# Kernel tuning notes

Measured on AMD Instinct MI355X. Metric: run time of the kernel, lower is better.

## Reference

```python
import jax, jax.numpy as jnp
import numpy as np
from jax import lax

EPS = 1e-8
NUM_CLASSES = 10
OUT_DIM = 16
IN_CAPS = 32 * 6 * 6  # 1152
IN_DIM = 8
NUM_ITERS = 3


def squash(x, axis=-1):
    norm = jnp.sum(x * x, axis=axis, keepdims=True)
    return norm / (norm + 1.0) * x / (jnp.sqrt(norm) + EPS)


def conv2d(x, w, b, stride):
    y = lax.conv_general_dilated(x, w, window_strides=(stride, stride), padding='VALID',
                                 dimension_numbers=('NCHW', 'OIHW', 'NCHW'))
    return y + b[None, :, None, None]


def setup_inputs() -> dict:
    key = jax.random.key(0)
    ks = jax.random.split(key, 12)
    B = 256
    inp = {}
    inp['x'] = jax.random.normal(ks[0], (B, 1, 28, 28), dtype=jnp.float32)
    inp['y'] = jax.random.randint(ks[1], (B,), 0, NUM_CLASSES)
    s = 0.05
    inp['conv1_w'] = jax.random.normal(ks[2], (256, 1, 9, 9), dtype=jnp.float32) * s
    inp['conv1_b'] = jnp.zeros((256,), dtype=jnp.float32)
    inp['prim_w'] = jax.random.normal(ks[3], (32 * 8, 256, 9, 9), dtype=jnp.float32) * s
    inp['prim_b'] = jnp.zeros((32 * 8,), dtype=jnp.float32)
    # torch init is randn; scaled down mildly for numerical sanity
    inp['route_W'] = jax.random.normal(ks[4], (NUM_CLASSES, IN_CAPS, IN_DIM, OUT_DIM), dtype=jnp.float32) * 0.1
    inp['dec_w1'] = jax.random.normal(ks[5], (NUM_CLASSES * OUT_DIM, 512), dtype=jnp.float32) * s
    inp['dec_b1'] = jnp.zeros((512,), dtype=jnp.float32)
    inp['dec_w2'] = jax.random.normal(ks[6], (512, 1024), dtype=jnp.float32) * s
    inp['dec_b2'] = jnp.zeros((1024,), dtype=jnp.float32)
    inp['dec_w3'] = jax.random.normal(ks[7], (1024, 28 * 28), dtype=jnp.float32) * s
    inp['dec_b3'] = jnp.zeros((28 * 28,), dtype=jnp.float32)
    return inp


def reference(x, y, conv1_w, conv1_b, prim_w, prim_b, route_W,
              dec_w1, dec_b1, dec_w2, dec_b2, dec_w3, dec_b3):
    B = x.shape[0]
    # conv1 + relu: [B,256,20,20]
    h = jax.nn.relu(conv2d(x, conv1_w, conv1_b, stride=1))
    # primary capsules: conv stride 2 -> [B,256,6,6] -> [B,1152,8], squash
    p = conv2d(h, prim_w, prim_b, stride=2)
    u = squash(p.reshape(B, -1, IN_DIM))  # [B,1152,8]
    # routing: u_hat [B,C,N,D]
    u_hat = jnp.einsum('bnd,cnde->bcne', u, route_W)
    b_logits = jnp.zeros_like(u_hat)
    for _ in range(NUM_ITERS - 1):
        c = jax.nn.softmax(b_logits, axis=2)
        s = jnp.sum(c * u_hat, axis=2, keepdims=True)  # [B,C,1,D]
        v = squash(s)
        b_logits = b_logits + u_hat * v
    c = jax.nn.softmax(b_logits, axis=2)
    s = jnp.sum(c * u_hat, axis=2, keepdims=True)
    v = squash(s)[:, :, 0, :]  # [B,C,D]
    logits = jax.nn.softmax(jnp.sqrt(jnp.sum(v * v, axis=-1)), axis=-1)  # [B,C]
    y_onehot = jax.nn.one_hot(y, NUM_CLASSES, dtype=v.dtype)  # [B,C]
    d = (v * y_onehot[:, :, None]).reshape(B, -1)  # [B,160]
    d = jax.nn.relu(d @ dec_w1 + dec_b1)
    d = jax.nn.relu(d @ dec_w2 + dec_b2)
    recons = d @ dec_w3 + dec_b3  # [B,784]
    return logits, recons
```

## Files before the change

### kernel.cpp

```cpp
#include <hip/hip_runtime.h>
#include <hip/hip_fp16.h>
#include <math.h>

#define EPS 1e-8f
#define AS1 __attribute__((address_space(1)))
#define AS3 __attribute__((address_space(3)))

typedef _Float16 f16x8 __attribute__((ext_vector_type(8)));
typedef float f32x4 __attribute__((ext_vector_type(4)));

__global__ __launch_bounds__(256) void transpose_k(const float* __restrict__ in,
                                                   float* __restrict__ out, int R, int C) {
    __shared__ float tile[64][65];
    int tx = threadIdx.x & 63, ty = threadIdx.x >> 6;
    int c0 = blockIdx.x * 64, r0 = blockIdx.y * 64;
#pragma unroll
    for (int i = 0; i < 16; ++i) {
        int r = r0 + ty + i * 4, c = c0 + tx;
        if (r < R && c < C) tile[ty + i * 4][tx] = in[(long)r * C + c];
    }
    __syncthreads();
#pragma unroll
    for (int i = 0; i < 16; ++i) {
        int r = c0 + ty + i * 4, c = r0 + tx;
        if (r < C && c < R) out[(long)r * R + c] = tile[tx][ty + i * 4];
    }
}

__global__ __launch_bounds__(256) void wprep_k(const float* __restrict__ prim_w,
                                               __half* __restrict__ w2) {
    __shared__ float pl[128 * 81];
    int t = threadIdx.x, co = blockIdx.x, cih = blockIdx.y;
    for (int i = t; i < 10368; i += 256) pl[i] = prim_w[co * 20736 + cih * 10368 + i];
    __syncthreads();
    for (int o = t; o < 10368; o += 256) {
        int tap = o >> 7, cil = o & 127;
        w2[(long)co * 20736 + tap * 256 + cih * 128 + cil] = __float2half(pl[cil * 81 + tap]);
    }
}

__global__ __launch_bounds__(256) void conv1_k(const float* __restrict__ x,
                                               const float* __restrict__ wt1,
                                               const float* __restrict__ bias,
                                               __half* __restrict__ hh) {
    __shared__ float img[784];
    __shared__ float wl2[81 * 128];
    int t = threadIdx.x, b = blockIdx.x;
    int chalf = blockIdx.y >> 1, ph = blockIdx.y & 1;
    for (int i = t; i < 784; i += 256) img[i] = x[b * 784 + i];
    for (int i = t; i < 81 * 128; i += 256) {
        int tap = i >> 7, j = i & 127;
        wl2[i] = wt1[tap * 256 + chalf * 128 + j];
    }
    __syncthreads();
    int lane = t & 63, grp = t >> 6;
    int col = lane * 2;
    float2 cb = *(const float2*)&bias[chalf * 128 + col];
    int ow0 = ph * 10;
    for (int oh = grp * 5; oh < grp * 5 + 5; ++oh) {
        float acc0[10], acc1[10];
#pragma unroll
        for (int p = 0; p < 10; ++p) { acc0[p] = 0.f; acc1[p] = 0.f; }
        for (int kh = 0; kh < 9; ++kh) {
            for (int kw = 0; kw < 9; ++kw) {
                float2 w2v = *(const float2*)&wl2[(kh * 9 + kw) * 128 + col];
                const float* irow = &img[(oh + kh) * 28 + ow0 + kw];
#pragma unroll
                for (int p = 0; p < 10; ++p) {
                    float iv = irow[p];
                    acc0[p] += iv * w2v.x;
                    acc1[p] += iv * w2v.y;
                }
            }
        }
#pragma unroll
        for (int p = 0; p < 10; ++p) {
            int pix = oh * 20 + ow0 + p;
            __half2 hv;
            hv.x = __float2half(fmaxf(acc0[p] + cb.x, 0.f));
            hv.y = __float2half(fmaxf(acc1[p] + cb.y, 0.f));
            *(__half2*)&hh[((long)b * 400 + pix) * 256 + chalf * 128 + col] = hv;
        }
    }
}

__global__ __launch_bounds__(256) void primgemm_k(const __half* __restrict__ hh,
                                                  const __half* __restrict__ w2,
                                                  float* __restrict__ Cpart) {
    __shared__ __align__(16) char lds[2][32768];
    const int t = threadIdx.x;
    const int lane = t & 63, w = t >> 6;
    const int l15 = lane & 15, kl = lane >> 4;
    const int sw = l15 & 7;

    const int bx = blockIdx.x;
    const int mt = bx >> 3, nb = (bx >> 2) & 1, ks = bx & 3;
    const int mr = w >> 1, nc = w & 1;

    long wsrc[4], asrc[4];
    int dstW[4];
#pragma unroll
    for (int q = 0; q < 4; ++q) {
        int row = q * 32 + w * 8 + (lane >> 3);
        int lc = (lane & 7) ^ (row & 7);
        dstW[q] = q * 4096 + w * 1024;
        wsrc[q] = (long)(nb * 128 + row) * 20736 + ks * 64 + lc * 8;
        int m = mt * 128 + row;
        int bi = m / 36, pos = m - bi * 36;
        int oy = pos / 6, ox = pos - oy * 6;
        asrc[q] = ((long)bi * 400 + oy * 40 + ox * 2) * 256 + ks * 64 + lc * 8;
    }

    f32x4 acc[4][4];
#pragma unroll
    for (int i = 0; i < 4; ++i)
#pragma unroll
        for (int j = 0; j < 4; ++j) acc[i][j] = (f32x4){0.f, 0.f, 0.f, 0.f};

    auto stage = [&](int bufi, int tap) {
        int kh = tap / 9, kw = tap - kh * 9;
        int woff = tap * 256;
        int aoff = (kh * 20 + kw) * 256;
#pragma unroll
        for (int q = 0; q < 4; ++q)
            __builtin_amdgcn_global_load_lds((const AS1 void*)(w2 + wsrc[q] + woff),
                                             (AS3 void*)(&lds[bufi][dstW[q]]), 16, 0, 0);
#pragma unroll
        for (int q = 0; q < 4; ++q)
            __builtin_amdgcn_global_load_lds((const AS1 void*)(hh + asrc[q] + aoff),
                                             (AS3 void*)(&lds[bufi][16384 + dstW[q]]), 16, 0, 0);
    };

    int wrowb[4], arowb[4], rdoff[2];
#pragma unroll
    for (int f = 0; f < 4; ++f) {
        wrowb[f] = (nc * 64 + f * 16 + l15) * 128;
        arowb[f] = 16384 + (mr * 64 + f * 16 + l15) * 128;
    }
#pragma unroll
    for (int kc = 0; kc < 2; ++kc) rdoff[kc] = ((kc * 4 + kl) ^ sw) << 4;

    stage(0, 0);
    __syncthreads();
    int buf = 0;
    for (int s = 0; s < 81; ++s) {
        if (s < 80) stage(buf ^ 1, s + 1);
        const char* B = lds[buf];
#pragma unroll
        for (int kc = 0; kc < 2; ++kc) {
            f16x8 wf[4], af[4];
#pragma unroll
            for (int nf = 0; nf < 4; ++nf) wf[nf] = *(const f16x8*)(B + wrowb[nf] + rdoff[kc]);
#pragma unroll
            for (int mf = 0; mf < 4; ++mf) af[mf] = *(const f16x8*)(B + arowb[mf] + rdoff[kc]);
#pragma unroll
            for (int mf = 0; mf < 4; ++mf)
#pragma unroll
                for (int nf = 0; nf < 4; ++nf)
                    acc[mf][nf] = __builtin_amdgcn_mfma_f32_16x16x32_f16(wf[nf], af[mf],
                                                                         acc[mf][nf], 0, 0, 0);
        }
        __syncthreads();
        buf ^= 1;
    }

    float* Cp = Cpart + (long)ks * 2359296;
#pragma unroll
    for (int mf = 0; mf < 4; ++mf)
#pragma unroll
        for (int nf = 0; nf < 4; ++nf) {
            int m = mt * 128 + mr * 64 + mf * 16 + l15;
            int co = nb * 128 + nc * 64 + nf * 16 + kl * 4;
            *(f32x4*)(Cp + (long)m * 256 + co) = acc[mf][nf];
        }
}

__global__ __launch_bounds__(256) void squashp_k(const float* __restrict__ Cpart,
                                                 const float* __restrict__ bias,
                                                 float* __restrict__ u) {
    __shared__ float sm[9216];
    __shared__ float bs[256];
    int t = threadIdx.x, b = blockIdx.x;
    bs[t] = bias[t];
    for (int i = t; i < 9216; i += 256) {
        float s = 0.f;
#pragma unroll
        for (int ks = 0; ks < 4; ++ks) s += Cpart[(long)ks * 2359296 + (long)b * 9216 + i];
        sm[i] = s;
    }
    __syncthreads();
    for (int cap = t; cap < 1152; cap += 256) {
        float xs[8], sn = 0.f;
#pragma unroll
        for (int d = 0; d < 8; ++d) {
            int f = cap * 8 + d;
            int co = f / 36, pos = f - co * 36;
            float vv = sm[pos * 256 + co] + bs[co];
            xs[d] = vv;
            sn += vv * vv;
        }
        float sc = sn / ((sn + 1.f) * (sqrtf(sn) + EPS));
#pragma unroll
        for (int d = 0; d < 8; ++d) u[(long)b * 9216 + cap * 8 + d] = xs[d] * sc;
    }
}

__global__ __launch_bounds__(256) void route_k(const float* __restrict__ u,
                                               const float* __restrict__ W,
                                               float* __restrict__ v) {
    __shared__ float red[4][18];
    int t = threadIdx.x;
    int c = blockIdx.x >> 8, b = blockIdx.x & 255;
    int lane = t & 63, w = t >> 6;
    const float* Wc = W + c * 147456;
    const float* ub = u + b * 9216;
    const float valid4 = (t < 128) ? 1.f : 0.f;

    float uh[5][16];
#pragma unroll
    for (int i = 0; i < 5; ++i) {
        int n = (i == 4) ? ((t < 128) ? 1024 + t : 0) : (t + 256 * i);
        float4 ua = *(const float4*)(ub + n * 8);
        float4 ubv = *(const float4*)(ub + n * 8 + 4);
        float ud[8] = {ua.x, ua.y, ua.z, ua.w, ubv.x, ubv.y, ubv.z, ubv.w};
#pragma unroll
        for (int e = 0; e < 16; ++e) uh[i][e] = 0.f;
#pragma unroll
        for (int d = 0; d < 8; ++d) {
            const float* wr = Wc + n * 128 + d * 16;
#pragma unroll
            for (int eq = 0; eq < 4; ++eq) {
                float4 wq = *(const float4*)(wr + eq * 4);
                uh[i][eq * 4 + 0] += ud[d] * wq.x;
                uh[i][eq * 4 + 1] += ud[d] * wq.y;
                uh[i][eq * 4 + 2] += ud[d] * wq.z;
                uh[i][eq * 4 + 3] += ud[d] * wq.w;
            }
        }
    }

    float vsum[16], sv[16];
#pragma unroll
    for (int e = 0; e < 16; ++e) vsum[e] = 0.f;

    for (int iter = 0; iter < 3; ++iter) {
        float li[5];
        float pmax = -1e30f;
#pragma unroll
        for (int i = 0; i < 5; ++i) {
            float s = 0.f;
#pragma unroll
            for (int e = 0; e < 16; ++e) s += uh[i][e] * vsum[e];
            li[i] = s;
            float sm = (i == 4 && valid4 == 0.f) ? -1e30f : s;
            pmax = fmaxf(pmax, sm);
        }
#pragma unroll
        for (int m = 1; m < 64; m <<= 1) pmax = fmaxf(pmax, __shfl_xor(pmax, m, 64));
        if (lane == 0) red[w][17] = pmax;
        __syncthreads();
        float M = fmaxf(fmaxf(red[0][17], red[1][17]), fmaxf(red[2][17], red[3][17]));

        float pe = 0.f, se[16];
#pragma unroll
        for (int e = 0; e < 16; ++e) se[e] = 0.f;
#pragma unroll
        for (int i = 0; i < 5; ++i) {
            float E = __expf(li[i] - M);
            if (i == 4) E *= valid4;
            pe += E;
#pragma unroll
            for (int e = 0; e < 16; ++e) se[e] += E * uh[i][e];
        }
#pragma unroll
        for (int m = 1; m < 64; m <<= 1) {
            pe += __shfl_xor(pe, m, 64);
#pragma unroll
            for (int e = 0; e < 16; ++e) se[e] += __shfl_xor(se[e], m, 64);
        }
        if (lane == 0) {
            red[w][16] = pe;
#pragma unroll
            for (int e = 0; e < 16; ++e) red[w][e] = se[e];
        }
        __syncthreads();
        float peT = red[0][16] + red[1][16] + red[2][16] + red[3][16];
        float rp = 1.f / peT;
        float nrm = 0.f;
#pragma unroll
        for (int e = 0; e < 16; ++e) {
            sv[e] = (red[0][e] + red[1][e] + red[2][e] + red[3][e]) * rp;
            nrm += sv[e] * sv[e];
        }
        float sc = nrm / ((nrm + 1.f) * (sqrtf(nrm) + EPS));
#pragma unroll
        for (int e = 0; e < 16; ++e) {
            sv[e] *= sc;
            vsum[e] += sv[e];
        }
    }
    if (t == 0) {
#pragma unroll
        for (int e = 0; e < 16; ++e) v[(b * 10 + c) * 16 + e] = sv[e];
    }
}

__global__ __launch_bounds__(256) void logits_k(const float* __restrict__ v,
                                                float* __restrict__ out) {
    int b = threadIdx.x;
    float nr[10];
#pragma unroll
    for (int c = 0; c < 10; ++c) {
        float s2 = 0.f;
#pragma unroll
        for (int e = 0; e < 16; ++e) {
            float xv = v[(b * 10 + c) * 16 + e];
            s2 += xv * xv;
        }
        nr[c] = sqrtf(s2);
    }
    float mx = nr[0];
#pragma unroll
    for (int c = 1; c < 10; ++c) mx = fmaxf(mx, nr[c]);
    float ex[10], sm = 0.f;
#pragma unroll
    for (int c = 0; c < 10; ++c) {
        ex[c] = __expf(nr[c] - mx);
        sm += ex[c];
    }
#pragma unroll
    for (int c = 0; c < 10; ++c) out[b * 10 + c] = ex[c] / sm;
}

__global__ __launch_bounds__(256) void fc1_k(const float* __restrict__ v,
                                             const int* __restrict__ y,
                                             const float* __restrict__ w1,
                                             const float* __restrict__ b1,
                                             float* __restrict__ h1) {
    int b = blockIdx.x, t = threadIdx.x;
    __shared__ float vs[16];
    int cls = y[b];
    if (t < 16) vs[t] = v[(b * 10 + cls) * 16 + t];
    __syncthreads();
    for (int j = t; j < 512; j += 256) {
        float a = b1[j];
#pragma unroll
        for (int d = 0; d < 16; ++d) a += vs[d] * w1[(cls * 16 + d) * 512 + j];
        h1[b * 512 + j] = fmaxf(a, 0.f);
    }
}

__global__ __launch_bounds__(256) void fc_k(const float* __restrict__ A,
                                            const float* __restrict__ Wt,
                                            const float* __restrict__ bias,
                                            float* __restrict__ C,
                                            int K, int N, int relu) {
    __shared__ float al[8 * 1024];
    int t = threadIdx.x;
    int j = blockIdx.x * 256 + t;
    int r0 = blockIdx.y * 8;
    for (int idx = t; idx < 8 * K; idx += 256) {
        int r = idx / K, kk = idx - r * K;
        al[r * K + kk] = A[(r0 + r) * K + kk];
    }
    __syncthreads();
    if (j < N) {
        float bj = bias[j];
        float acc[8];
#pragma unroll
        for (int i = 0; i < 8; ++i) acc[i] = bj;
        for (int k = 0; k < K; ++k) {
            float w = Wt[(long)k * N + j];
#pragma unroll
            for (int i = 0; i < 8; ++i) acc[i] += al[i * K + k] * w;
        }
#pragma unroll
        for (int i = 0; i < 8; ++i) {
            float o = acc[i];
            if (relu) o = fmaxf(o, 0.f);
            C[(r0 + i) * N + j] = o;
        }
    }
}

extern "C" void kernel_launch(void* const* d_in, const int* in_sizes, int n_in,
                              void* d_out, int out_size, void* d_ws, size_t ws_size,
                              hipStream_t stream) {
    (void)in_sizes; (void)n_in; (void)out_size; (void)ws_size;
    const float* x       = (const float*)d_in[0];
    const int*   y       = (const int*)d_in[1];
    const float* conv1_w = (const float*)d_in[2];
    const float* conv1_b = (const float*)d_in[3];
    const float* prim_w  = (const float*)d_in[4];
    const float* prim_b  = (const float*)d_in[5];
    const float* route_W = (const float*)d_in[6];
    const float* dec_w1  = (const float*)d_in[7];
    const float* dec_b1  = (const float*)d_in[8];
    const float* dec_w2  = (const float*)d_in[9];
    const float* dec_b2  = (const float*)d_in[10];
    const float* dec_w3  = (const float*)d_in[11];
    const float* dec_b3  = (const float*)d_in[12];
    float* out = (float*)d_out;

    float* ws  = (float*)d_ws;
    float* Cp  = ws;
    float* u   = Cp + 9437184;
    float* wt1 = u + 2359296;
    float* v   = wt1 + 20736;
    float* h1  = v + 40960;
    float* h2  = h1 + 131072;
    __half* hh = (__half*)(h2 + 262144);
    __half* w2 = hh + 26214400;

    hipLaunchKernelGGL(transpose_k, dim3(2, 4), dim3(256), 0, stream, conv1_w, wt1, 256, 81);
    hipLaunchKernelGGL(wprep_k, dim3(256, 2), dim3(256), 0, stream, prim_w, w2);
    hipLaunchKernelGGL(conv1_k, dim3(256, 4), dim3(256), 0, stream, x, wt1, conv1_b, hh);
    hipLaunchKernelGGL(primgemm_k, dim3(576), dim3(256), 0, stream, hh, w2, Cp);
    hipLaunchKernelGGL(squashp_k, dim3(256), dim3(256), 0, stream, Cp, prim_b, u);
    hipLaunchKernelGGL(route_k, dim3(2560), dim3(256), 0, stream, u, route_W, v);
    hipLaunchKernelGGL(logits_k, dim3(1), dim3(256), 0, stream, v, out);
    hipLaunchKernelGGL(fc1_k, dim3(256), dim3(256), 0, stream, v, y, dec_w1, dec_b1, h1);
    hipLaunchKernelGGL(fc_k, dim3(4, 32), dim3(256), 0, stream, h1, dec_w2, dec_b2, h2, 512, 1024, 1);
    hipLaunchKernelGGL(fc_k, dim3(4, 32), dim3(256), 0, stream, h2, dec_w3, dec_b3, out + 2560, 1024, 784, 0);
}
```

Before: 696.8 us.

## Split routing into u_hat precompute kernel with fp16 storage; register-cache conv1 rows

Routing is split in two. A new kernel computes u_hat once per (class, capsule group), keeping W in LDS and reusing it across all batch items, and writes u_hat as fp16 into the reused hh buffer. The routing kernel then just loads its fp16 u_hat slice instead of re-reading W from global memory for every batch item. Conv1 also loads each input row into 19 registers once and reuses them across kw taps instead of re-reading LDS. The costs are a 47 MB fp16 intermediate written and read through HBM, fp16 rounding of u_hat, and an extra barrier per routing iteration.

```diff
diff --git a/kernel.cpp b/kernel.cpp
--- a/kernel.cpp
+++ b/kernel.cpp
@@ -61,15 +61,19 @@
         float acc0[10], acc1[10];
 #pragma unroll
         for (int p = 0; p < 10; ++p) { acc0[p] = 0.f; acc1[p] = 0.f; }
+#pragma unroll
         for (int kh = 0; kh < 9; ++kh) {
+            float r[19];
+            const float* irow = &img[(oh + kh) * 28 + ow0];
+#pragma unroll
+            for (int q = 0; q < 19; ++q) r[q] = irow[q];
+#pragma unroll
             for (int kw = 0; kw < 9; ++kw) {
-                float2 w2v = *(const float2*)&wl2[(kh * 9 + kw) * 128 + col];
-                const float* irow = &img[(oh + kh) * 28 + ow0 + kw];
+                float2 wv = *(const float2*)&wl2[(kh * 9 + kw) * 128 + col];
 #pragma unroll
                 for (int p = 0; p < 10; ++p) {
-                    float iv = irow[p];
-                    acc0[p] += iv * w2v.x;
-                    acc1[p] += iv * w2v.y;
+                    acc0[p] += r[kw + p] * wv.x;
+                    acc1[p] += r[kw + p] * wv.y;
                 }
             }
         }
@@ -205,38 +209,69 @@
     }
 }
 
-__global__ __launch_bounds__(256) void route_k(const float* __restrict__ u,
-                                               const float* __restrict__ W,
-                                               float* __restrict__ v) {
+__global__ __launch_bounds__(256) void uhat_k(const float* __restrict__ u,
+                                              const float* __restrict__ W,
+                                              __half* __restrict__ uh) {
+    __shared__ float wl[32 * 132];
+    int t = threadIdx.x;
+    int c = blockIdx.x / 36, ng = blockIdx.x - c * 36;
+    const float* Wc = W + (long)c * 147456 + ng * 4096;
+    for (int i = t; i < 4096; i += 256) {
+        int row = i >> 7, k = i & 127;
+        wl[row * 132 + k] = Wc[i];
+    }
+    __syncthreads();
+    int nl = t >> 3, bl = t & 7;
+    int n = ng * 32 + nl;
+    const float* wr = &wl[nl * 132];
+    for (int bq = 0; bq < 32; ++bq) {
+        int b = bq * 8 + bl;
+        const float* ub = u + (long)b * 9216 + n * 8;
+        float4 ua = *(const float4*)ub, uv = *(const float4*)(ub + 4);
+        float ud[8] = {ua.x, ua.y, ua.z, ua.w, uv.x, uv.y, uv.z, uv.w};
+        float acc[16];
+#pragma unroll
+        for (int e = 0; e < 16; ++e) acc[e] = 0.f;
+#pragma unroll
+        for (int d = 0; d < 8; ++d) {
+            const float* wd = wr + d * 16;
+#pragma unroll
+            for (int eq = 0; eq < 4; ++eq) {
+                float4 wq = *(const float4*)(wd + eq * 4);
+                acc[eq * 4 + 0] += ud[d] * wq.x;
+                acc[eq * 4 + 1] += ud[d] * wq.y;
+                acc[eq * 4 + 2] += ud[d] * wq.z;
+                acc[eq * 4 + 3] += ud[d] * wq.w;
+            }
+        }
+        f16x8 o0, o1;
+#pragma unroll
+        for (int e = 0; e < 8; ++e) {
+            o0[e] = (_Float16)acc[e];
+            o1[e] = (_Float16)acc[8 + e];
+        }
+        __half* dst = uh + ((long)(c * 256 + b)) * 18432 + n * 16;
+        *(f16x8*)dst = o0;
+        *(f16x8*)(dst + 8) = o1;
+    }
+}
+
+__global__ __launch_bounds__(256) void route2_k(const __half* __restrict__ uh,
+                                                float* __restrict__ v) {
     __shared__ float red[4][18];
     int t = threadIdx.x;
     int c = blockIdx.x >> 8, b = blockIdx.x & 255;
     int lane = t & 63, w = t >> 6;
-    const float* Wc = W + c * 147456;
-    const float* ub = u + b * 9216;
     const float valid4 = (t < 128) ? 1.f : 0.f;
-
-    float uh[5][16];
+    const __half* ub = uh + ((long)(c * 256 + b)) * 18432;
+
+    f16x8 uhh[5][2];
 #pragma unroll
     for (int i = 0; i < 5; ++i) {
         int n = (i == 4) ? ((t < 128) ? 1024 + t : 0) : (t + 256 * i);
-        float4 ua = *(const float4*)(ub + n * 8);
-        float4 ubv = *(const float4*)(ub + n * 8 + 4);
-        float ud[8] = {ua.x, ua.y, ua.z, ua.w, ubv.x, ubv.y, ubv.z, ubv.w};
-#pragma unroll
-        for (int e = 0; e < 16; ++e) uh[i][e] = 0.f;
-#pragma unroll
-        for (int d = 0; d < 8; ++d) {
-            const float* wr = Wc + n * 128 + d * 16;
-#pragma unroll
-            for (int eq = 0; eq < 4; ++eq) {
-                float4 wq = *(const float4*)(wr + eq * 4);
-                uh[i][eq * 4 + 0] += ud[d] * wq.x;
-                uh[i][eq * 4 + 1] += ud[d] * wq.y;
-                uh[i][eq * 4 + 2] += ud[d] * wq.z;
-                uh[i][eq * 4 + 3] += ud[d] * wq.w;
-            }
-        }
+        const __half* p = ub + n * 16;
+        uhh[i][0] = *(const f16x8*)p;
+        uhh[i][1] = *(const f16x8*)(p + 8);
     }
 
     float vsum[16], sv[16];
@@ -250,7 +285,7 @@
         for (int i = 0; i < 5; ++i) {
             float s = 0.f;
 #pragma unroll
-            for (int e = 0; e < 16; ++e) s += uh[i][e] * vsum[e];
+            for (int e = 0; e < 16; ++e) s += (float)uhh[i][e >> 3][e & 7] * vsum[e];
             li[i] = s;
             float sm = (i == 4 && valid4 == 0.f) ? -1e30f : s;
             pmax = fmaxf(pmax, sm);
@@ -270,7 +305,7 @@
             if (i == 4) E *= valid4;
             pe += E;
 #pragma unroll
-            for (int e = 0; e < 16; ++e) se[e] += E * uh[i][e];
+            for (int e = 0; e < 16; ++e) se[e] += E * (float)uhh[i][e >> 3][e & 7];
         }
 #pragma unroll
         for (int m = 1; m < 64; m <<= 1) {
@@ -298,6 +333,7 @@
             sv[e] *= sc;
             vsum[e] += sv[e];
         }
+        __syncthreads();
     }
     if (t == 0) {
 #pragma unroll
@@ -411,13 +447,15 @@
     float* h2  = h1 + 131072;
     __half* hh = (__half*)(h2 + 262144);
     __half* w2 = hh + 26214400;
+    __half* uhb = hh;
 
     hipLaunchKernelGGL(transpose_k, dim3(2, 4), dim3(256), 0, stream, conv1_w, wt1, 256, 81);
     hipLaunchKernelGGL(wprep_k, dim3(256, 2), dim3(256), 0, stream, prim_w, w2);
     hipLaunchKernelGGL(conv1_k, dim3(256, 4), dim3(256), 0, stream, x, wt1, conv1_b, hh);
     hipLaunchKernelGGL(primgemm_k, dim3(576), dim3(256), 0, stream, hh, w2, Cp);
     hipLaunchKernelGGL(squashp_k, dim3(256), dim3(256), 0, stream, Cp, prim_b, u);
-    hipLaunchKernelGGL(route_k, dim3(2560), dim3(256), 0, stream, u, route_W, v);
+    hipLaunchKernelGGL(uhat_k, dim3(360), dim3(256), 0, stream, u, route_W, uhb);
+    hipLaunchKernelGGL(route2_k, dim3(2560), dim3(256), 0, stream, uhb, v);
     hipLaunchKernelGGL(logits_k, dim3(1), dim3(256), 0, stream, v, out);
     hipLaunchKernelGGL(fc1_k, dim3(256), dim3(256), 0, stream, v, y, dec_w1, dec_b1, h1);
     hipLaunchKernelGGL(fc_k, dim3(4, 32), dim3(256), 0, stream, h1, dec_w2, dec_b2, h2, 512, 1024, 1);
```

New measurement: 581.3 us. -16.6%, faster.
